# Optimization experiments

Measured on AMD Instinct MI355X. Metric: run time of the kernel, lower is better.

Reference implementation:

```python
import jax, jax.numpy as jnp
import numpy as np

B, T, D, H = 64, 2048, 128, 256  # batch, time, input features, num_cells


def setup_inputs() -> dict:
    key = jax.random.key(0)
    ks = jax.random.split(key, 8)
    w = lambda k, shape: (jax.random.normal(k, shape, dtype=jnp.float32) * 0.05)
    return {
        "x": jax.random.normal(ks[0], (B, T, D), dtype=jnp.float32),
        "k_fwd": w(ks[1], (D, 4 * H)),
        "r_fwd": w(ks[2], (H, 4 * H)),
        "b_fwd": jnp.zeros((4 * H,), jnp.float32),
        "k_bwd": w(ks[3], (D, 4 * H)),
        "r_bwd": w(ks[4], (H, 4 * H)),
        "b_bwd": jnp.zeros((4 * H,), jnp.float32),
        "att_w": jax.random.uniform(ks[5], (H,), dtype=jnp.float32),
    }


def _lstm(x, kernel, rec, bias):
    """Keras-style LSTM (gate order i,f,c,o), return_sequences=True. x: [B,T,D] -> [B,T,H]."""
    xw = jnp.einsum('btd,dk->btk', x, kernel) + bias  # precompute input contribution [B,T,4H]
    h0 = jnp.zeros((x.shape[0], rec.shape[0]), x.dtype)

    def step(carry, xw_t):
        h, c = carry
        z = xw_t + h @ rec  # [B,4H]
        i, f, g, o = jnp.split(z, 4, axis=-1)
        c = jax.nn.sigmoid(f) * c + jax.nn.sigmoid(i) * jnp.tanh(g)
        h = jax.nn.sigmoid(o) * jnp.tanh(c)
        return (h, c), h

    _, hs = jax.lax.scan(step, (h0, h0), jnp.swapaxes(xw, 0, 1))  # hs: [T,B,H]
    return jnp.swapaxes(hs, 0, 1)


def reference(x, k_fwd, r_fwd, b_fwd, k_bwd, r_bwd, b_bwd, att_w):
    # Bidirectional LSTM, merge_mode='sum'
    h_f = _lstm(x, k_fwd, r_fwd, b_fwd)
    h_b = _lstm(x[:, ::-1], k_bwd, r_bwd, b_bwd)[:, ::-1]
    h = h_f + h_b  # [B,T,H]
    # Additive attention pooling (dropout identity at inference)
    m = jnp.tanh(h)
    a = jax.nn.softmax(jnp.einsum('h,bth->bt', att_w, m), axis=-1)  # [B,T]
    r = jnp.einsum('bth,bt->bh', h, a)  # [B,H]
    return jnp.tanh(r)
```

## Files before the change

### kernel.cpp

```cpp
#include <hip/hip_runtime.h>
#include <cstdint>
#include <cstddef>

#define TT 2048
#define DD 128
#define HH 256
#define G4 1024

typedef _Float16 half4_t __attribute__((ext_vector_type(4)));
typedef _Float16 half8_t __attribute__((ext_vector_type(8)));
typedef float floatx4 __attribute__((ext_vector_type(4)));

union H4U64 { uint64_t u; half4_t h; };
union H8U64x2 { uint64_t u[2]; half8_t h; };

__device__ __forceinline__ float sigm(float x) { return 1.f / (1.f + __expf(-x)); }
__device__ __forceinline__ float tanh_f(float x) { return 1.f - 2.f / (1.f + __expf(2.f * x)); }

__device__ __forceinline__ half8_t cvt8(float4 a, float4 b) {
  half8_t v;
  v[0] = (_Float16)a.x; v[1] = (_Float16)a.y; v[2] = (_Float16)a.z; v[3] = (_Float16)a.w;
  v[4] = (_Float16)b.x; v[5] = (_Float16)b.y; v[6] = (_Float16)b.z; v[7] = (_Float16)b.w;
  return v;
}

__global__ void prep_kernel(const float* __restrict__ rf, const float* __restrict__ rb,
                            const float* __restrict__ kf, const float* __restrict__ kb,
                            _Float16* __restrict__ RT, _Float16* __restrict__ KT) {
  int idx = blockIdx.x * 256 + threadIdx.x;
  if (idx < 2 * G4 * HH) {
    int dir = idx >> 18, k = (idx >> 10) & 255, n = idx & 1023;
    const float* src = dir ? rb : rf;
    RT[((size_t)(dir * G4 + n)) * HH + k] = (_Float16)src[(size_t)k * G4 + n];
  } else {
    int i2 = idx - 2 * G4 * HH;
    int dir = i2 >> 17, k = (i2 >> 10) & 127, n = i2 & 1023;
    const float* src = dir ? kb : kf;
    KT[((size_t)(dir * G4 + n)) * DD + k] = (_Float16)src[(size_t)k * G4 + n];
  }
}


__global__ __launch_bounds__(256, 1) void lstm_rec_kernel(
    const float* __restrict__ x,
    const float* __restrict__ bias_f, const float* __restrict__ bias_b,
    const _Float16* __restrict__ RT, const _Float16* __restrict__ KT,
    uint64_t* __restrict__ ring, int* __restrict__ flags,
    _Float16* __restrict__ hseq) {
  const int bid = blockIdx.x;
  const int split = bid >> 3;
  const int g = bid & 7;
  const int dir = g >> 2;
  const int bg = g & 3;
  const int tid = threadIdx.x;
  const int w = tid >> 6, lane = tid & 63;
  const int lo16 = lane & 15, q = lane >> 4;

  __shared__ _Float16 tile[2][64][20];

  const float* __restrict__ bias = dir ? bias_b : bias_f;

  half8_t bR[4][8], bK[4][4];
  float bgate[4];
#pragma unroll
  for (int gate = 0; gate < 4; ++gate) {
    const int col = gate * 256 + split * 64 + w * 16 + lo16;
    const _Float16* bp = RT + (size_t)(dir * G4 + col) * HH + q * 8;
#pragma unroll
    for (int kk = 0; kk < 8; ++kk) bR[gate][kk] = *reinterpret_cast<const half8_t*>(bp + kk * 32);
    const _Float16* kp = KT + (size_t)(dir * G4 + col) * DD + q * 8;
#pragma unroll
    for (int kx = 0; kx < 4; ++kx) bK[gate][kx] = *reinterpret_cast<const half8_t*>(kp + kx * 32);
    bgate[gate] = bias[col];
  }

  const float* __restrict__ xrow = x + ((size_t)(bg * 16 + lo16) * TT) * DD;
  int* __restrict__ flagG = flags + g * 32;

  const int kgl  = tid >> 5;
  const int tb   = (tid >> 1) & 15;
  const int part = tid & 1;
  const int kg_global = split * 8 + kgl;
  const int hofs = split * 64 + kgl * 8 + part * 4;

  float c[4] = {0.f, 0.f, 0.f, 0.f};

  int tx = dir ? TT - 1 : 0;
  float4 xr[8];
  {
    const float* xp = xrow + (size_t)tx * DD + q * 8;
#pragma unroll
    for (int kx = 0; kx < 4; ++kx) {
      xr[2 * kx]     = *reinterpret_cast<const float4*>(xp + kx * 32);
      xr[2 * kx + 1] = *reinterpret_cast<const float4*>(xp + kx * 32 + 4);
    }
  }
  half8_t ax[4];
#pragma unroll
  for (int kx = 0; kx < 4; ++kx) ax[kx] = cvt8(xr[2 * kx], xr[2 * kx + 1]);

  for (int s = 0; s < TT; ++s) {
    tx = dir ? (TT - 1 - s) : s;

    {
      const int sn = (s + 1 < TT) ? s + 1 : s;
      const int txn = dir ? (TT - 1 - sn) : sn;
      const float* xp = xrow + (size_t)txn * DD + q * 8;
#pragma unroll
      for (int kx = 0; kx < 4; ++kx) {
        xr[2 * kx]     = *reinterpret_cast<const float4*>(xp + kx * 32);
        xr[2 * kx + 1] = *reinterpret_cast<const float4*>(xp + kx * 32 + 4);
      }
    }

    floatx4 acc[4];
#pragma unroll
    for (int gate = 0; gate < 4; ++gate) acc[gate] = floatx4{0.f, 0.f, 0.f, 0.f};

    half8_t ah[8];
    if (s > 0) {
      while (true) {
        int v = __hip_atomic_load(&flagG[lane & 15], __ATOMIC_RELAXED, __HIP_MEMORY_SCOPE_AGENT);
        if (__all(v >= s)) break;
        __builtin_amdgcn_s_sleep(1);
      }
      asm volatile("" ::: "memory");

      const uint64_t* rs = ring + ((size_t)(((s - 1) & 3) * 8 + g)) * 1024;
#pragma unroll
      for (int kk = 0; kk < 8; ++kk) {
        H8U64x2 u;
        const uint64_t* p = rs + (size_t)(((kk * 4 + q) * 16 + lo16) * 2);
        u.u[0] = __hip_atomic_load((uint64_t*)(p),     __ATOMIC_RELAXED, __HIP_MEMORY_SCOPE_AGENT);
        u.u[1] = __hip_atomic_load((uint64_t*)(p + 1), __ATOMIC_RELAXED, __HIP_MEMORY_SCOPE_AGENT);
        ah[kk] = u.h;
      }
    }

#pragma unroll
    for (int kx = 0; kx < 4; ++kx)
#pragma unroll
      for (int gate = 0; gate < 4; ++gate)
        acc[gate] = __builtin_amdgcn_mfma_f32_16x16x32_f16(ax[kx], bK[gate][kx], acc[gate], 0, 0, 0);

    if (s > 0) {
#pragma unroll
      for (int kk = 0; kk < 8; ++kk)
#pragma unroll
        for (int gate = 0; gate < 4; ++gate)
          acc[gate] = __builtin_amdgcn_mfma_f32_16x16x32_f16(ah[kk], bR[gate][kk], acc[gate], 0, 0, 0);
    }

    const int par = s & 1;
    {
      half4_t hv4;
#pragma unroll
      for (int r = 0; r < 4; ++r) {
        const float zi = acc[0][r] + bgate[0];
        const float zf = acc[1][r] + bgate[1];
        const float zg = acc[2][r] + bgate[2];
        const float zo = acc[3][r] + bgate[3];
        c[r] = sigm(zf) * c[r] + sigm(zi) * tanh_f(zg);
        hv4[r] = (_Float16)(sigm(zo) * tanh_f(c[r]));
      }
      *reinterpret_cast<half4_t*>(&tile[par][w * 16 + lo16][q * 4]) = hv4;
    }
    __syncthreads();

    {
      H4U64 val;
#pragma unroll
      for (int j = 0; j < 4; ++j) val.h[j] = tile[par][kgl * 8 + part * 4 + j][tb];
      uint64_t* rp = ring + ((size_t)((s & 3) * 8 + g)) * 1024 + (kg_global * 16 + tb) * 2 + part;
      __hip_atomic_store(rp, val.u, __ATOMIC_RELAXED, __HIP_MEMORY_SCOPE_AGENT);

      asm volatile("s_waitcnt vmcnt(0)" ::: "memory");
      if ((tid & 63) == 0) {
        __hip_atomic_store(&flagG[split * 4 + w], s + 1, __ATOMIC_RELAXED, __HIP_MEMORY_SCOPE_AGENT);
      }

      *reinterpret_cast<uint64_t*>(hseq + ((size_t)g * TT + tx) * (16 * HH) + (size_t)tb * HH + hofs) = val.u;
    }

#pragma unroll
    for (int kx = 0; kx < 4; ++kx) ax[kx] = cvt8(xr[2 * kx], xr[2 * kx + 1]);
  }
}


__global__ __launch_bounds__(256) void attn_kernel(const _Float16* __restrict__ h_ex,
                                                   const float* __restrict__ att_w,
                                                   float* __restrict__ out) {
  const int b = blockIdx.x;
  const int bg = b >> 4, b16 = b & 15;
  const int tid = threadIdx.x;
  const int w = tid >> 6, lane = tid & 63;
  __shared__ float sc[TT];
  __shared__ float red[8];
  const size_t ST = 16 * HH;
  const _Float16* __restrict__ hf = h_ex + (size_t)bg * TT * ST + b16 * HH;
  const _Float16* __restrict__ hb = h_ex + (size_t)(4 + bg) * TT * ST + b16 * HH;

  const int h0 = lane * 4;
  const float aw0 = att_w[h0], aw1 = att_w[h0 + 1], aw2 = att_w[h0 + 2], aw3 = att_w[h0 + 3];

  for (int t = w; t < TT; t += 4) {
    half4_t f4 = *reinterpret_cast<const half4_t*>(hf + (size_t)t * ST + h0);
    half4_t b4 = *reinterpret_cast<const half4_t*>(hb + (size_t)t * ST + h0);
    float s = aw0 * tanh_f((float)f4[0] + (float)b4[0])
            + aw1 * tanh_f((float)f4[1] + (float)b4[1])
            + aw2 * tanh_f((float)f4[2] + (float)b4[2])
            + aw3 * tanh_f((float)f4[3] + (float)b4[3]);
#pragma unroll
    for (int off = 32; off >= 1; off >>= 1) s += __shfl_xor(s, off);
    if (lane == 0) sc[t] = s;
  }
  __syncthreads();

  float m = -1e30f;
  for (int i = tid; i < TT; i += 256) m = fmaxf(m, sc[i]);
#pragma unroll
  for (int off = 32; off >= 1; off >>= 1) m = fmaxf(m, __shfl_xor(m, off));
  if (lane == 0) red[w] = m;
  __syncthreads();
  m = fmaxf(fmaxf(red[0], red[1]), fmaxf(red[2], red[3]));

  float ssum = 0.f;
  for (int i = tid; i < TT; i += 256) {
    float e = __expf(sc[i] - m);
    sc[i] = e;
    ssum += e;
  }
#pragma unroll
  for (int off = 32; off >= 1; off >>= 1) ssum += __shfl_xor(ssum, off);
  if (lane == 0) red[4 + w] = ssum;
  __syncthreads();
  const float inv = 1.f / (red[4] + red[5] + red[6] + red[7]);

  float r = 0.f;
  const _Float16* pf = hf + tid;
  const _Float16* pb = hb + tid;
  for (int t = 0; t < TT; ++t)
    r += sc[t] * ((float)pf[(size_t)t * ST] + (float)pb[(size_t)t * ST]);
  out[b * HH + tid] = tanh_f(r * inv);
}


extern "C" void kernel_launch(void* const* d_in, const int* in_sizes, int n_in,
                              void* d_out, int out_size, void* d_ws, size_t ws_size,
                              hipStream_t stream) {
  const float* x     = (const float*)d_in[0];
  const float* k_fwd = (const float*)d_in[1];
  const float* r_fwd = (const float*)d_in[2];
  const float* b_fwd = (const float*)d_in[3];
  const float* k_bwd = (const float*)d_in[4];
  const float* r_bwd = (const float*)d_in[5];
  const float* b_bwd = (const float*)d_in[6];
  const float* att_w = (const float*)d_in[7];
  float* out = (float*)d_out;

  const size_t RT_bytes   = (size_t)2 * G4 * HH * sizeof(_Float16);
  const size_t KT_bytes   = (size_t)2 * G4 * DD * sizeof(_Float16);
  const size_t flag_bytes = (size_t)8 * 32 * sizeof(int);
  const size_t ring_bytes = (size_t)4 * 8 * 1024 * sizeof(uint64_t);
  char* ws = (char*)d_ws;
  _Float16* RT    = (_Float16*)ws;
  _Float16* KT    = (_Float16*)(ws + RT_bytes);
  int*      flags = (int*)(ws + RT_bytes + KT_bytes);
  uint64_t* ring  = (uint64_t*)(ws + RT_bytes + KT_bytes + flag_bytes);
  _Float16* hseq  = (_Float16*)(ws + RT_bytes + KT_bytes + flag_bytes + ring_bytes);

  hipMemsetAsync(flags, 0, flag_bytes, stream);
  hipLaunchKernelGGL(prep_kernel, dim3(3072), dim3(256), 0, stream,
                     r_fwd, r_bwd, k_fwd, k_bwd, RT, KT);
  hipLaunchKernelGGL(lstm_rec_kernel, dim3(32), dim3(256), 0, stream,
                     x, b_fwd, b_bwd, RT, KT, ring, flags, hseq);
  hipLaunchKernelGGL(attn_kernel, dim3(64), dim3(256), 0, stream, hseq, att_w, out);
}
```

Measured before the change: 7.554 ms.

## Replace flag-based ring handoff with sentinel-polled hidden-state sequence buffer

```diff
diff --git a/kernel.cpp b/kernel.cpp
--- a/kernel.cpp
+++ b/kernel.cpp
@@ -41,11 +41,12 @@
 }
 
 
+#define SENT 0xFFFFFFFFFFFFFFFFull
+
 __global__ __launch_bounds__(256, 1) void lstm_rec_kernel(
     const float* __restrict__ x,
     const float* __restrict__ bias_f, const float* __restrict__ bias_b,
     const _Float16* __restrict__ RT, const _Float16* __restrict__ KT,
-    uint64_t* __restrict__ ring, int* __restrict__ flags,
     _Float16* __restrict__ hseq) {
   const int bid = blockIdx.x;
   const int split = bid >> 3;
@@ -75,13 +76,14 @@
   }
 
   const float* __restrict__ xrow = x + ((size_t)(bg * 16 + lo16) * TT) * DD;
-  int* __restrict__ flagG = flags + g * 32;
 
   const int kgl  = tid >> 5;
   const int tb   = (tid >> 1) & 15;
   const int part = tid & 1;
-  const int kg_global = split * 8 + kgl;
-  const int hofs = split * 64 + kgl * 8 + part * 4;
+  const int hofsq = split * 16 + kgl * 2 + part;
+
+  uint64_t* __restrict__ hq = (uint64_t*)hseq;
+  const size_t gbase = (size_t)g * TT;
 
   float c[4] = {0.f, 0.f, 0.f, 0.f};
 
@@ -102,6 +104,18 @@
   for (int s = 0; s < TT; ++s) {
     tx = dir ? (TT - 1 - s) : s;
 
+    uint64_t g0[8], g1[8];
+    const uint64_t* gp = hq;
+    if (s > 0) {
+      const int txp = dir ? (TT - s) : (s - 1);
+      gp = hq + (gbase + txp) * 1024 + (size_t)(lo16 * 64 + q * 2);
+#pragma unroll
+      for (int kk = 0; kk < 8; ++kk) {
+        g0[kk] = __hip_atomic_load(gp + kk * 8,     __ATOMIC_RELAXED, __HIP_MEMORY_SCOPE_AGENT);
+        g1[kk] = __hip_atomic_load(gp + kk * 8 + 1, __ATOMIC_RELAXED, __HIP_MEMORY_SCOPE_AGENT);
+      }
+    }
+
     {
       const int sn = (s + 1 < TT) ? s + 1 : s;
       const int txn = dir ? (TT - 1 - sn) : sn;
@@ -117,38 +131,35 @@
 #pragma unroll
     for (int gate = 0; gate < 4; ++gate) acc[gate] = floatx4{0.f, 0.f, 0.f, 0.f};
 
-    half8_t ah[8];
+#pragma unroll
+    for (int kx = 0; kx < 4; ++kx)
+#pragma unroll
+      for (int gate = 0; gate < 4; ++gate)
+        acc[gate] = __builtin_amdgcn_mfma_f32_16x16x32_f16(ax[kx], bK[gate][kx], acc[gate], 0, 0, 0);
+
     if (s > 0) {
       while (true) {
-        int v = __hip_atomic_load(&flagG[lane & 15], __ATOMIC_RELAXED, __HIP_MEMORY_SCOPE_AGENT);
-        if (__all(v >= s)) break;
-        __builtin_amdgcn_s_sleep(1);
-      }
-      asm volatile("" ::: "memory");
-
-      const uint64_t* rs = ring + ((size_t)(((s - 1) & 3) * 8 + g)) * 1024;
+        bool ok = true;
+#pragma unroll
+        for (int kk = 0; kk < 8; ++kk) ok = ok & (g0[kk] != SENT) & (g1[kk] != SENT);
+        if (__all(ok)) break;
+#pragma unroll
+        for (int kk = 0; kk < 8; ++kk) {
+          if (g0[kk] == SENT)
+            g0[kk] = __hip_atomic_load(gp + kk * 8,     __ATOMIC_RELAXED, __HIP_MEMORY_SCOPE_AGENT);
+          if (g1[kk] == SENT)
+            g1[kk] = __hip_atomic_load(gp + kk * 8 + 1, __ATOMIC_RELAXED, __HIP_MEMORY_SCOPE_AGENT);
+        }
+      }
 #pragma unroll
       for (int kk = 0; kk < 8; ++kk) {
         H8U64x2 u;
-        const uint64_t* p = rs + (size_t)(((kk * 4 + q) * 16 + lo16) * 2);
-        u.u[0] = __hip_atomic_load((uint64_t*)(p),     __ATOMIC_RELAXED, __HIP_MEMORY_SCOPE_AGENT);
-        u.u[1] = __hip_atomic_load((uint64_t*)(p + 1), __ATOMIC_RELAXED, __HIP_MEMORY_SCOPE_AGENT);
-        ah[kk] = u.h;
-      }
-    }
-
-#pragma unroll
-    for (int kx = 0; kx < 4; ++kx)
-#pragma unroll
-      for (int gate = 0; gate < 4; ++gate)
-        acc[gate] = __builtin_amdgcn_mfma_f32_16x16x32_f16(ax[kx], bK[gate][kx], acc[gate], 0, 0, 0);
-
-    if (s > 0) {
-#pragma unroll
-      for (int kk = 0; kk < 8; ++kk)
+        u.u[0] = g0[kk];
+        u.u[1] = g1[kk];
 #pragma unroll
         for (int gate = 0; gate < 4; ++gate)
-          acc[gate] = __builtin_amdgcn_mfma_f32_16x16x32_f16(ah[kk], bR[gate][kk], acc[gate], 0, 0, 0);
+          acc[gate] = __builtin_amdgcn_mfma_f32_16x16x32_f16(u.h, bR[gate][kk], acc[gate], 0, 0, 0);
+      }
     }
 
     const int par = s & 1;
@@ -171,15 +182,8 @@
       H4U64 val;
 #pragma unroll
       for (int j = 0; j < 4; ++j) val.h[j] = tile[par][kgl * 8 + part * 4 + j][tb];
-      uint64_t* rp = ring + ((size_t)((s & 3) * 8 + g)) * 1024 + (kg_global * 16 + tb) * 2 + part;
-      __hip_atomic_store(rp, val.u, __ATOMIC_RELAXED, __HIP_MEMORY_SCOPE_AGENT);
-
-      asm volatile("s_waitcnt vmcnt(0)" ::: "memory");
-      if ((tid & 63) == 0) {
-        __hip_atomic_store(&flagG[split * 4 + w], s + 1, __ATOMIC_RELAXED, __HIP_MEMORY_SCOPE_AGENT);
-      }
-
-      *reinterpret_cast<uint64_t*>(hseq + ((size_t)g * TT + tx) * (16 * HH) + (size_t)tb * HH + hofs) = val.u;
+      __hip_atomic_store(hq + (gbase + tx) * 1024 + (size_t)(tb * 64 + hofsq), val.u,
+                         __ATOMIC_RELAXED, __HIP_MEMORY_SCOPE_AGENT);
     }
 
 #pragma unroll
@@ -261,19 +265,16 @@
 
   const size_t RT_bytes   = (size_t)2 * G4 * HH * sizeof(_Float16);
   const size_t KT_bytes   = (size_t)2 * G4 * DD * sizeof(_Float16);
-  const size_t flag_bytes = (size_t)8 * 32 * sizeof(int);
-  const size_t ring_bytes = (size_t)4 * 8 * 1024 * sizeof(uint64_t);
+  const size_t hseq_bytes = (size_t)8 * TT * 16 * HH * sizeof(_Float16);
   char* ws = (char*)d_ws;
-  _Float16* RT    = (_Float16*)ws;
-  _Float16* KT    = (_Float16*)(ws + RT_bytes);
-  int*      flags = (int*)(ws + RT_bytes + KT_bytes);
-  uint64_t* ring  = (uint64_t*)(ws + RT_bytes + KT_bytes + flag_bytes);
-  _Float16* hseq  = (_Float16*)(ws + RT_bytes + KT_bytes + flag_bytes + ring_bytes);
-
-  hipMemsetAsync(flags, 0, flag_bytes, stream);
+  _Float16* RT   = (_Float16*)ws;
+  _Float16* KT   = (_Float16*)(ws + RT_bytes);
+  _Float16* hseq = (_Float16*)(ws + RT_bytes + KT_bytes);
+
+  hipMemsetAsync(hseq, 0xFF, hseq_bytes, stream);
   hipLaunchKernelGGL(prep_kernel, dim3(3072), dim3(256), 0, stream,
                      r_fwd, r_bwd, k_fwd, k_bwd, RT, KT);
   hipLaunchKernelGGL(lstm_rec_kernel, dim3(32), dim3(256), 0, stream,
-                     x, b_fwd, b_bwd, RT, KT, ring, flags, hseq);
+                     x, b_fwd, b_bwd, RT, KT, hseq);
   hipLaunchKernelGGL(attn_kernel, dim3(64), dim3(256), 0, stream, hseq, att_w, out);
 }
```

Result: slower. 10.06 ms (+33.2%).
